# Performance work log

Hardware: AMD Instinct MI355X
Metric: run time of the kernel (lower is better)

Reference implementation:

```python
import jax, jax.numpy as jnp
import numpy as np

L, H, C, HS, V, BS = 4, 4, 1024, 256, 32000, 1024  # layers, heads, n_embd, head_size, vocab, block_size
B, T = 4, 1024
EPS = 1e-5

def _ln(x, g, b):
    mu = jnp.mean(x, axis=-1, keepdims=True)
    var = jnp.mean((x - mu) ** 2, axis=-1, keepdims=True)
    return (x - mu) / jnp.sqrt(var + EPS) * g + b

def setup_inputs() -> dict:
    key = jax.random.key(0)
    ks = iter(jax.random.split(key, 32))
    s = 0.02
    inp = {
        'idx': jax.random.randint(next(ks), (B, T), 0, V),
        'tok_emb': jax.random.normal(next(ks), (V, C), jnp.float32) * s,
        'pos_emb': jax.random.normal(next(ks), (BS, C), jnp.float32) * s,
        'wq': jax.random.normal(next(ks), (L, H, C, HS), jnp.float32) * s,
        'wk': jax.random.normal(next(ks), (L, H, C, HS), jnp.float32) * s,
        'wv': jax.random.normal(next(ks), (L, H, C, HS), jnp.float32) * s,
        'proj_w': jax.random.normal(next(ks), (L, C, C), jnp.float32) * s,
        'proj_b': jnp.zeros((L, C), jnp.float32),
        'ln1_g': jnp.ones((L, C), jnp.float32),
        'ln1_b': jnp.zeros((L, C), jnp.float32),
        'ln2_g': jnp.ones((L, C), jnp.float32),
        'ln2_b': jnp.zeros((L, C), jnp.float32),
        'ff_w1': jax.random.normal(next(ks), (L, C, 4 * C), jnp.float32) * s,
        'ff_b1': jnp.zeros((L, 4 * C), jnp.float32),
        'ff_w2': jax.random.normal(next(ks), (L, 4 * C, C), jnp.float32) * s,
        'ff_b2': jnp.zeros((L, C), jnp.float32),
        'lnf_g': jnp.ones((C,), jnp.float32),
        'lnf_b': jnp.zeros((C,), jnp.float32),
        'head_w': jax.random.normal(next(ks), (C, V), jnp.float32) * s,
        'head_b': jnp.zeros((V,), jnp.float32),
    }
    return inp

def reference(idx, tok_emb, pos_emb, wq, wk, wv, proj_w, proj_b, ln1_g, ln1_b,
              ln2_g, ln2_b, ff_w1, ff_b1, ff_w2, ff_b2, lnf_g, lnf_b, head_w, head_b):
    b, t = idx.shape
    x = tok_emb[idx] + pos_emb[:t]  # (B,T,C)
    causal = jnp.tril(jnp.ones((t, t), bool))
    inv_sqrt_c = np.float32(1.0 / np.sqrt(C))  # NOTE: original scales by sqrt(n_embd), not head_size
    for l in range(L):
        xn = _ln(x, ln1_g[l], ln1_b[l])
        q = jnp.einsum('btc,hcd->bhtd', xn, wq[l])
        k = jnp.einsum('bsc,hcd->bhsd', xn, wk[l])
        v = jnp.einsum('bsc,hcd->bhsd', xn, wv[l])
        scores = jnp.einsum('bhtd,bhsd->bhts', q, k)
        scores = jnp.where(causal, scores, -jnp.inf) * inv_sqrt_c
        # original: F.softmax(xdot, dim=1) on (B,T,T) -> normalize over the QUERY axis
        alpha = jax.nn.softmax(scores, axis=2)
        y = jnp.einsum('bhts,bhsd->bhtd', alpha, v)
        y = y.transpose(0, 2, 1, 3).reshape(b, t, C)  # concat heads
        x = x + y @ proj_w[l] + proj_b[l]
        xn2 = _ln(x, ln2_g[l], ln2_b[l])
        h = jax.nn.relu(xn2 @ ff_w1[l] + ff_b1[l])
        x = x + h @ ff_w2[l] + ff_b2[l]
    x = _ln(x, lnf_g, lnf_b)
    logits = x @ head_w + head_b  # (B,T,V)
    return logits
```

## Files before the change

### kernel.cpp

```cpp
#include <hip/hip_runtime.h>


#define C_  1024
#define T_  1024
#define HS_ 256
#define H_  4
#define L_  4
#define V_  32000
#define B_  4
#define M_  4096

typedef __attribute__((ext_vector_type(8))) short  bfx8;
typedef __attribute__((ext_vector_type(4))) float  fx4;
typedef __attribute__((ext_vector_type(4))) unsigned short usx4;

__device__ __forceinline__ unsigned short f2bf(float f) {
  unsigned int u = __builtin_bit_cast(unsigned int, f);
  u += 0x7fffu + ((u >> 16) & 1u);
  return (unsigned short)(u >> 16);
}
__device__ __forceinline__ float bf2f(unsigned short u) {
  return __builtin_bit_cast(float, ((unsigned int)u) << 16);
}

__device__ __forceinline__ void gload16(const unsigned short* g, unsigned short* l) {
  __builtin_amdgcn_global_load_lds(
      (const __attribute__((address_space(1))) unsigned int*)g,
      (__attribute__((address_space(3))) unsigned int*)l, 16, 0, 0);
}

template<int BIAS, int RES, int RELU, int OUTBF>
__global__ __launch_bounds__(256, 2) void gemm_bf16(
    const unsigned short* __restrict__ A, const unsigned short* __restrict__ Bm,
    const float* __restrict__ bias, const float* __restrict__ res,
    void* __restrict__ out,
    int M, int N, int K, int lda, int ldb, int ldc,
    long sA, long sB, long sC1, long sC2, int zShift, long rowOuter)
{
  __shared__ unsigned short As[128 * 32];
  __shared__ unsigned short Bs[128 * 32];
  const int z = blockIdx.z;
  A  += (long)z * sA;
  Bm += (long)z * sB;
  const long outOff = ((long)(z >> zShift)) * sC1 + (long)(z & ((1 << zShift) - 1)) * sC2;
  const int m0 = blockIdx.x * 128, n0 = blockIdx.y * 128;
  const int tid = threadIdx.x;
  const int lane = tid & 63, wave = tid >> 6;
  const int wm = (wave >> 1) * 64, wn = (wave & 1) * 64;
  const int fr = lane & 15, kb = lane >> 4;
  const int sr = lane >> 2;
  const int csw = (((lane & 3) ^ ((lane >> 3) & 3)) << 3);
  const int aco = ((kb ^ ((lane >> 1) & 3)) << 3);

  fx4 acc[4][4] = {};

  for (int k0 = 0; k0 < K; k0 += 32) {
    #pragma unroll
    for (int i = 0; i < 2; ++i) {
      const int c = wave * 2 + i;
      gload16(A  + (long)(m0 + c * 16 + sr) * lda + k0 + csw, &As[c * 512]);
      gload16(Bm + (long)(n0 + c * 16 + sr) * ldb + k0 + csw, &Bs[c * 512]);
    }
    __syncthreads();
    bfx8 af[4], bf[4];
    #pragma unroll
    for (int i = 0; i < 4; ++i)
      af[i] = *reinterpret_cast<const bfx8*>(&As[(wm + i * 16 + fr) * 32 + aco]);
    #pragma unroll
    for (int j = 0; j < 4; ++j)
      bf[j] = *reinterpret_cast<const bfx8*>(&Bs[(wn + j * 16 + fr) * 32 + aco]);
    #pragma unroll
    for (int i = 0; i < 4; ++i)
      #pragma unroll
      for (int j = 0; j < 4; ++j)
        acc[i][j] = __builtin_amdgcn_mfma_f32_16x16x32_bf16(af[i], bf[j], acc[i][j], 0, 0, 0);
    __syncthreads();
  }

  const float* resp = res;
  if (RES) resp += outOff;
  const int rbase = (lane >> 4) * 4;
  #pragma unroll
  for (int j = 0; j < 4; ++j) {
    const int n = n0 + wn + j * 16 + fr;
    float bv = 0.f;
    if (BIAS) bv = bias[n];
    #pragma unroll
    for (int i = 0; i < 4; ++i) {
      #pragma unroll
      for (int r = 0; r < 4; ++r) {
        const int m = m0 + wm + i * 16 + rbase + r;
        const long off = outOff + ((long)(m >> 10)) * rowOuter + (long)(m & 1023) * ldc + n;
        float val = acc[i][j][r] + bv;
        if (RELU) val = fmaxf(val, 0.f);
        if (RES) val += resp[((long)(m >> 10)) * rowOuter + (long)(m & 1023) * ldc + n];
        if (OUTBF) ((unsigned short*)out)[off] = f2bf(val);
        else       ((float*)out)[off] = val;
      }
    }
  }
}

#define BAR() __builtin_amdgcn_s_barrier()
#define LGKM() { asm volatile("s_waitcnt lgkmcnt(0)" ::: "memory"); \
                 __builtin_amdgcn_sched_barrier(0); }
#define VM8()  asm volatile("s_waitcnt vmcnt(8)" ::: "memory")
#define STA(tau, kh) { const int tc = (tau) < NT ? (tau) : NT - 1; \
  const unsigned short* src = A + (long)(m0 + wave * 16 + srow) * lda + tc * 64 + (kh) * 32 + csw; \
  unsigned short* d = &S[(((tau) & 1) * 2 + (kh)) * 8192 + wave * 512]; \
  gload16(src, d); gload16(src + (long)128 * lda, d + 4096); }
#define STB(tau, kh) { const int tc = (tau) < NT ? (tau) : NT - 1; \
  const unsigned short* src = Bm + (long)(n0 + wave * 16 + srow) * ldb + tc * 64 + (kh) * 32 + csw; \
  unsigned short* d = &S[32768 + (((tau) & 1) * 2 + (kh)) * 8192 + wave * 512]; \
  gload16(src, d); gload16(src + (long)128 * ldb, d + 4096); }
#define RDA(dst, par, kh, rh) { _Pragma("unroll") for (int i = 0; i < 4; ++i) \
  dst[i] = *reinterpret_cast<const bfx8*>(&S[((par)*2+(kh))*8192 + (wr*128 + (rh)*64 + i*16 + fr)*32 + aco]); }
#define RDB(dst, par, kh) { _Pragma("unroll") for (int j = 0; j < 4; ++j) \
  dst[j] = *reinterpret_cast<const bfx8*>(&S[32768 + ((par)*2+(kh))*8192 + (wc*64 + j*16 + fr)*32 + aco]); }
#define MM(rh, afx, bfx) { __builtin_amdgcn_s_setprio(1); \
  _Pragma("unroll") for (int i = 0; i < 4; ++i) { _Pragma("unroll") for (int j = 0; j < 4; ++j) \
    acc[(rh)*4+i][j] = __builtin_amdgcn_mfma_f32_16x16x32_bf16(afx[i], bfx[j], acc[(rh)*4+i][j], 0, 0, 0); } \
  __builtin_amdgcn_s_setprio(0); }

template<int BIAS, int RELU, int OUTBF, int EPI>
__global__ __launch_bounds__(512, 2) void gemm256(
    const unsigned short* __restrict__ A, const unsigned short* __restrict__ Bm,
    const float* __restrict__ bias, void* __restrict__ out,
    int K, int lda, int ldb, int ldc,
    long sA, long sB, long sC1, long rowOuter)
{
  __shared__ unsigned short S[65536];
  const int z = blockIdx.z;
  A  += (long)z * sA;
  Bm += (long)z * sB;
  const long outOff = (long)z * sC1;
  const int m0 = blockIdx.x * 256, n0 = blockIdx.y * 256;
  const int tid = threadIdx.x;
  const int lane = tid & 63, wave = tid >> 6;
  const int wr = wave >> 2, wc = wave & 3;
  const int fr = lane & 15, kb = lane >> 4;
  const int srow = lane >> 2;
  const int csw = (((lane & 3) ^ (((lane >> 5) & 1) << 1)) << 3);
  const int aco = ((kb ^ (((fr >> 3) & 1) << 1)) << 3);
  const int NT = K >> 6;
  const int NI = NT >> 1;

  fx4 acc[8][4] = {};
  bfx8 afa[4], afb[4], bf0[4], bf1[4];

  STB(0, 0); STA(0, 0); STB(0, 1); STA(0, 1);
  STB(1, 0); STA(1, 0); STB(1, 1); STA(1, 1);
  VM8();
  BAR();
  RDA(afa, 0, 0, 0); RDB(bf1, 0, 0);
  LGKM();
  BAR();

  for (int t = 0; t < NI; ++t) {
    const int u = 2 * t;
    STB(u + 2, 0); RDA(afb, 0, 0, 1);                 MM(0, afa, bf1); LGKM(); BAR();
    STA(u + 2, 0); RDA(afa, 0, 1, 0); RDB(bf0, 0, 1); MM(1, afb, bf1); LGKM(); VM8(); BAR();
    STB(u + 2, 1); RDA(afb, 0, 1, 1);                 MM(0, afa, bf0); LGKM(); BAR();
    STA(u + 2, 1); RDA(afa, 1, 0, 0); RDB(bf1, 1, 0); MM(1, afb, bf0); LGKM(); VM8(); BAR();
    STB(u + 3, 0); RDA(afb, 1, 0, 1);                 MM(0, afa, bf1); LGKM(); BAR();
    STA(u + 3, 0); RDA(afa, 1, 1, 0); RDB(bf0, 1, 1); MM(1, afb, bf1); LGKM(); VM8(); BAR();
    STB(u + 3, 1); RDA(afb, 1, 1, 1);                 MM(0, afa, bf0); LGKM(); BAR();
    STA(u + 3, 1); RDA(afa, 0, 0, 0); RDB(bf1, 0, 0); MM(1, afb, bf0); LGKM(); VM8(); BAR();
  }
  asm volatile("s_waitcnt vmcnt(0)" ::: "memory");
  BAR();

  const int rbase = (lane >> 4) * 4;
  if (EPI == 1) {
    const int sel = n0 >> 10, h = (n0 >> 8) & 3;
    unsigned short* dst = (unsigned short*)out
        + (long)sel * ((long)B_ * H_ * T_ * HS_) + (long)h * T_ * HS_;
    #pragma unroll
    for (int j = 0; j < 4; ++j) {
      const int d = wc * 64 + j * 16 + fr;
      #pragma unroll
      for (int i = 0; i < 8; ++i) {
        #pragma unroll
        for (int r = 0; r < 4; ++r) {
          const int m = m0 + wr * 128 + i * 16 + rbase + r;
          const int bq = m >> 10, tq = m & 1023;
          dst[(long)bq * H_ * T_ * HS_ + (long)tq * HS_ + d] = f2bf(acc[i][j][r]);
        }
      }
    }
  } else {
    float* lf = (float*)S;
    #pragma unroll
    for (int jh = 0; jh < 2; ++jh) {
      #pragma unroll
      for (int jj = 0; jj < 2; ++jj)
        #pragma unroll
        for (int i = 0; i < 8; ++i)
          #pragma unroll
          for (int r = 0; r < 4; ++r) {
            const int row = i * 16 + rbase + r;
            const int cw = (jj * 16 + fr) ^ ((row & 7) << 2);
            lf[wave * 4096 + row * 32 + cw] = acc[i][jh * 2 + jj][r];
          }
      #pragma unroll
      for (int rs = 0; rs < 16; ++rs) {
        const int row = rs * 8 + (lane >> 3);
        const int c0 = (lane & 7) * 4;
        const int cw = c0 ^ ((row & 7) << 2);
        fx4 val = *reinterpret_cast<const fx4*>(&lf[wave * 4096 + row * 32 + cw]);
        const int n = n0 + wc * 64 + jh * 32 + c0;
        const int m = m0 + wr * 128 + row;
        const long off = outOff + ((long)(m >> 10)) * rowOuter + (long)(m & 1023) * ldc + n;
        if (BIAS) {
          const float4 bb = *reinterpret_cast<const float4*>(bias + n);
          val[0] += bb.x; val[1] += bb.y; val[2] += bb.z; val[3] += bb.w;
        }
        if (RELU) {
          val[0] = fmaxf(val[0], 0.f); val[1] = fmaxf(val[1], 0.f);
          val[2] = fmaxf(val[2], 0.f); val[3] = fmaxf(val[3], 0.f);
        }
        if (OUTBF) {
          usx4 o = { f2bf(val[0]), f2bf(val[1]), f2bf(val[2]), f2bf(val[3]) };
          *reinterpret_cast<usx4*>((unsigned short*)out + off) = o;
        } else {
          *reinterpret_cast<float4*>((float*)out + off) = *(const float4*)&val;
        }
      }
      __builtin_amdgcn_sched_barrier(0);
    }
  }
}

template<typename TIN>
__global__ __launch_bounds__(256) void transpose_k(const TIN* __restrict__ src,
    unsigned short* __restrict__ dst, int R, int Cc, int zShiftT, long sOuter) {
  __shared__ float ts[64][65];
  const long zb = blockIdx.z;
  src += zb * (long)R * Cc;
  dst += (zb >> zShiftT) * sOuter + (zb & ((1 << zShiftT) - 1)) * ((long)R * Cc);
  const int r0 = blockIdx.y * 64, c0 = blockIdx.x * 64;
  const int tr = threadIdx.x >> 4;
  const int tc = (threadIdx.x & 15) * 4;
  #pragma unroll
  for (int it = 0; it < 4; ++it) {
    const int r = tr + it * 16;
    float4 v;
    if constexpr (sizeof(TIN) == 4) {
      v = *reinterpret_cast<const float4*>(src + (long)(r0 + r) * Cc + c0 + tc);
    } else {
      usx4 u = *reinterpret_cast<const usx4*>(src + (long)(r0 + r) * Cc + c0 + tc);
      v.x = bf2f(u[0]); v.y = bf2f(u[1]); v.z = bf2f(u[2]); v.w = bf2f(u[3]);
    }
    ts[r][tc + 0] = v.x; ts[r][tc + 1] = v.y; ts[r][tc + 2] = v.z; ts[r][tc + 3] = v.w;
  }
  __syncthreads();
  #pragma unroll
  for (int it = 0; it < 4; ++it) {
    const int cj = tr + it * 16;
    usx4 o = { f2bf(ts[tc + 0][cj]), f2bf(ts[tc + 1][cj]),
               f2bf(ts[tc + 2][cj]), f2bf(ts[tc + 3][cj]) };
    *reinterpret_cast<usx4*>(dst + (long)(c0 + cj) * R + r0 + tc) = o;
  }
}

__global__ __launch_bounds__(256) void embed_k(const int* __restrict__ idx,
                                               const float* __restrict__ tok,
                                               const float* __restrict__ pos,
                                               float* __restrict__ x) {
  const int row = blockIdx.x;
  const int t = row & (T_ - 1);
  const int id = idx[row];
  const int c = threadIdx.x * 4;
  const float4 a = *reinterpret_cast<const float4*>(tok + (long)id * C_ + c);
  const float4 p = *reinterpret_cast<const float4*>(pos + (long)t * C_ + c);
  float4 ov = { a.x + p.x, a.y + p.y, a.z + p.z, a.w + p.w };
  *reinterpret_cast<float4*>(x + (long)row * C_ + c) = ov;
}

__global__ __launch_bounds__(256) void ln_k(const float* __restrict__ x,
                                            const float* __restrict__ g,
                                            const float* __restrict__ b,
                                            unsigned short* __restrict__ o) {
  __shared__ float red[8];
  const int row = blockIdx.x;
  const int c = threadIdx.x * 4;
  const float4 v = *reinterpret_cast<const float4*>(x + (long)row * C_ + c);
  float s1 = v.x + v.y + v.z + v.w;
  float s2 = v.x * v.x + v.y * v.y + v.z * v.z + v.w * v.w;
  #pragma unroll
  for (int off = 32; off; off >>= 1) {
    s1 += __shfl_xor(s1, off, 64);
    s2 += __shfl_xor(s2, off, 64);
  }
  const int lane = threadIdx.x & 63, w = threadIdx.x >> 6;
  if (lane == 0) { red[w] = s1; red[4 + w] = s2; }
  __syncthreads();
  s1 = red[0] + red[1] + red[2] + red[3];
  s2 = red[4] + red[5] + red[6] + red[7];
  const float mu = s1 * (1.f / C_);
  float var = s2 * (1.f / C_) - mu * mu;
  var = fmaxf(var, 0.f);
  const float inv = rsqrtf(var + 1e-5f);
  const float4 gg = *reinterpret_cast<const float4*>(g + c);
  const float4 bb = *reinterpret_cast<const float4*>(b + c);
  usx4 ov;
  ov[0] = f2bf((v.x - mu) * inv * gg.x + bb.x);
  ov[1] = f2bf((v.y - mu) * inv * gg.y + bb.y);
  ov[2] = f2bf((v.z - mu) * inv * gg.z + bb.z);
  ov[3] = f2bf((v.w - mu) * inv * gg.w + bb.w);
  *reinterpret_cast<usx4*>(o + (long)row * C_ + c) = ov;
}

__global__ __launch_bounds__(256) void colsm_k(const unsigned short* __restrict__ a,
                                               unsigned short* __restrict__ aT) {
  __shared__ float red[8];
  const int row = blockIdx.x;
  const int s = row & (T_ - 1);
  const unsigned short* p = a + (long)row * T_;
  const int t0 = threadIdx.x * 4;
  const usx4 u = *reinterpret_cast<const usx4*>(p + t0);
  const float scale = 0.03125f;
  float vals[4];
  float m = -1e30f;
  #pragma unroll
  for (int j = 0; j < 4; ++j) {
    vals[j] = (t0 + j >= s) ? bf2f(u[j]) * scale : -1e30f;
    m = fmaxf(m, vals[j]);
  }
  #pragma unroll
  for (int off = 32; off; off >>= 1) m = fmaxf(m, __shfl_xor(m, off, 64));
  const int lane = threadIdx.x & 63, w = threadIdx.x >> 6;
  if (lane == 0) red[w] = m;
  __syncthreads();
  m = fmaxf(fmaxf(red[0], red[1]), fmaxf(red[2], red[3]));
  __syncthreads();
  float e[4], sum = 0.f;
  #pragma unroll
  for (int j = 0; j < 4; ++j) {
    e[j] = (t0 + j >= s) ? __expf(vals[j] - m) : 0.f;
    sum += e[j];
  }
  #pragma unroll
  for (int off = 32; off; off >>= 1) sum += __shfl_xor(sum, off, 64);
  if (lane == 0) red[w] = sum;
  __syncthreads();
  sum = red[0] + red[1] + red[2] + red[3];
  const float inv = 1.f / sum;
  usx4 ov = { f2bf(e[0] * inv), f2bf(e[1] * inv), f2bf(e[2] * inv), f2bf(e[3] * inv) };
  *reinterpret_cast<usx4*>(aT + (long)row * T_ + t0) = ov;
}

extern "C" void kernel_launch(void* const* d_in, const int* in_sizes, int n_in,
                              void* d_out, int out_size, void* d_ws, size_t ws_size,
                              hipStream_t stream) {
  const int*   idx    = (const int*)d_in[0];
  const float* tok    = (const float*)d_in[1];
  const float* pos    = (const float*)d_in[2];
  const float* wq     = (const float*)d_in[3];
  const float* wk     = (const float*)d_in[4];
  const float* wv     = (const float*)d_in[5];
  const float* proj_w = (const float*)d_in[6];
  const float* proj_b = (const float*)d_in[7];
  const float* ln1_g  = (const float*)d_in[8];
  const float* ln1_b  = (const float*)d_in[9];
  const float* ln2_g  = (const float*)d_in[10];
  const float* ln2_b  = (const float*)d_in[11];
  const float* ff_w1  = (const float*)d_in[12];
  const float* ff_b1  = (const float*)d_in[13];
  const float* ff_w2  = (const float*)d_in[14];
  const float* ff_b2  = (const float*)d_in[15];
  const float* lnf_g  = (const float*)d_in[16];
  const float* lnf_b  = (const float*)d_in[17];
  const float* head_w = (const float*)d_in[18];
  const float* head_b = (const float*)d_in[19];
  float* outp = (float*)d_out;

  typedef unsigned short us;
  char* w = (char*)d_ws;
  float* x    = (float*)(w + 0);
  us* xn      = (us*)(w + 16777216);
  us* qkv     = (us*)(w + 25165824);
  us* kptr    = qkv + 4194304;
  us* vptr    = qkv + 8388608;
  us* vT      = (us*)(w + 50331648);
  us* yc      = (us*)(w + 58720256);
  us* sc      = (us*)(w + 67108864);
  us* headT   = (us*)(w + 67108864);
  us* alpha   = (us*)(w + 100663296);
  us* aT      = (us*)(w + 134217728);
  us* hidden  = aT;
  us* wqkvT   = (us*)(w + 167772160);
  us* projT   = (us*)(w + 192937984);
  us* ff1T    = (us*)(w + 201326592);
  us* ff2T    = (us*)(w + 234881024);
  if (ws_size < (size_t)268435456) return;

  const long HHC = (long)H_ * HS_ * C_;
  transpose_k<float><<<dim3(HS_/64, C_/64, L_*H_), 256, 0, stream>>>(wq, wqkvT,           C_, HS_, 2, 3*HHC);
  transpose_k<float><<<dim3(HS_/64, C_/64, L_*H_), 256, 0, stream>>>(wk, wqkvT + HHC,     C_, HS_, 2, 3*HHC);
  transpose_k<float><<<dim3(HS_/64, C_/64, L_*H_), 256, 0, stream>>>(wv, wqkvT + 2*HHC,   C_, HS_, 2, 3*HHC);
  transpose_k<float><<<dim3(C_/64, C_/64, L_), 256, 0, stream>>>(proj_w, projT, C_, C_, 0, (long)C_*C_);
  transpose_k<float><<<dim3(4*C_/64, C_/64, L_), 256, 0, stream>>>(ff_w1, ff1T, C_, 4*C_, 0, (long)C_*4*C_);
  transpose_k<float><<<dim3(C_/64, 4*C_/64, L_), 256, 0, stream>>>(ff_w2, ff2T, 4*C_, C_, 0, (long)4*C_*C_);

  embed_k<<<M_, 256, 0, stream>>>(idx, tok, pos, x);

  for (int l = 0; l < L_; ++l) {
    ln_k<<<M_, 256, 0, stream>>>(x, ln1_g + l * C_, ln1_b + l * C_, xn);

    dim3 gqkv(M_/256, 3*C_/256, 1);
    gemm256<0,0,1,1><<<gqkv, 512, 0, stream>>>(xn, wqkvT + l * 3 * HHC, nullptr, qkv,
        C_, C_, C_, 0, 0, 0, 0, 0);

    dim3 gs(T_/256, T_/256, B_*H_);
    gemm256<0,0,1,0><<<gs, 512, 0, stream>>>(kptr, qkv, nullptr, sc,
        HS_, HS_, HS_, T_, (long)T_*HS_, (long)T_*HS_, (long)T_*T_, 0);

    colsm_k<<<B_*H_*T_, 256, 0, stream>>>(sc, aT);

    transpose_k<us><<<dim3(T_/64, T_/64, B_*H_), 256, 0, stream>>>(aT, alpha, T_, T_, 0, (long)T_*T_);
    transpose_k<us><<<dim3(HS_/64, T_/64, B_*H_), 256, 0, stream>>>(vptr, vT, T_, HS_, 0, (long)T_*HS_);

    dim3 gp(T_/128, HS_/128, B_*H_);
    gemm_bf16<0,0,0,1><<<gp, 256, 0, stream>>>(alpha, vT, nullptr, nullptr, yc,
        T_, HS_, T_, T_, T_, C_, (long)T_*T_, (long)HS_*T_, (long)T_*C_, HS_, 2, (long)T_*C_);

    dim3 gj(M_/128, C_/128, 1);
    gemm_bf16<1,1,0,0><<<gj, 256, 0, stream>>>(yc, projT + (long)l*C_*C_, proj_b + l*C_, x, x,
        M_, C_, C_, C_, C_, C_, 0, 0, 0, 0, 0, (long)T_*C_);

    ln_k<<<M_, 256, 0, stream>>>(x, ln2_g + l * C_, ln2_b + l * C_, xn);

    dim3 g1(M_/256, 4*C_/256, 1);
    gemm256<1,1,1,0><<<g1, 512, 0, stream>>>(xn, ff1T + (long)l*4*C_*C_, ff_b1 + (long)l*4*C_,
        hidden, C_, C_, C_, 4*C_, 0, 0, 0, (long)1024*4*C_);

    dim3 g2(M_/128, C_/128, 1);
    gemm_bf16<1,1,0,0><<<g2, 256, 0, stream>>>(hidden, ff2T + (long)l*C_*4*C_, ff_b2 + l*C_, x, x,
        M_, C_, 4*C_, 4*C_, 4*C_, C_, 0, 0, 0, 0, 0, (long)T_*C_);
  }

  ln_k<<<M_, 256, 0, stream>>>(x, lnf_g, lnf_b, xn);

  transpose_k<float><<<dim3(V_/64, C_/64, 1), 256, 0, stream>>>(head_w, headT, C_, V_, 0, (long)C_*V_);

  dim3 gh(M_/256, V_/256, 1);
  gemm256<1,0,0,0><<<gh, 512, 0, stream>>>(xn, headT, head_b, outp,
      C_, C_, C_, V_, 0, 0, 0, (long)1024*V_);
}
```

Measured before the change: 1.605 ms.

## Fuse column softmax with transpose and stage QKV epilogue through LDS

```diff
diff --git a/kernel.cpp b/kernel.cpp
--- a/kernel.cpp
+++ b/kernel.cpp
@@ -13,6 +13,7 @@
 typedef __attribute__((ext_vector_type(8))) short  bfx8;
 typedef __attribute__((ext_vector_type(4))) float  fx4;
 typedef __attribute__((ext_vector_type(4))) unsigned short usx4;
+typedef __attribute__((ext_vector_type(8))) unsigned short usx8;
 
 __device__ __forceinline__ unsigned short f2bf(float f) {
   unsigned int u = __builtin_bit_cast(unsigned int, f);
@@ -126,8 +127,7 @@
 __global__ __launch_bounds__(512, 2) void gemm256(
     const unsigned short* __restrict__ A, const unsigned short* __restrict__ Bm,
     const float* __restrict__ bias, void* __restrict__ out,
-    int K, int lda, int ldb, int ldc,
-    long sA, long sB, long sC1, long rowOuter)
+    int K, int lda, int ldb, int ldc, long sA, long sB, long sC1)
 {
   __shared__ unsigned short S[65536];
   const int z = blockIdx.z;
@@ -171,63 +171,56 @@
   BAR();
 
   const int rbase = (lane >> 4) * 4;
+  unsigned short* dst1 = nullptr;
   if (EPI == 1) {
     const int sel = n0 >> 10, h = (n0 >> 8) & 3;
-    unsigned short* dst = (unsigned short*)out
-        + (long)sel * ((long)B_ * H_ * T_ * HS_) + (long)h * T_ * HS_;
-    #pragma unroll
-    for (int j = 0; j < 4; ++j) {
-      const int d = wc * 64 + j * 16 + fr;
+    const int bq = m0 >> 10, tq0 = m0 & 1023;
+    dst1 = (unsigned short*)out + ((long)sel * B_ + bq) * H_ * T_ * HS_
+         + (long)h * T_ * HS_ + (long)tq0 * HS_;
+  }
+  float* lf = (float*)S;
+  #pragma unroll
+  for (int jh = 0; jh < 2; ++jh) {
+    #pragma unroll
+    for (int jj = 0; jj < 2; ++jj)
       #pragma unroll
-      for (int i = 0; i < 8; ++i) {
+      for (int i = 0; i < 8; ++i)
         #pragma unroll
         for (int r = 0; r < 4; ++r) {
-          const int m = m0 + wr * 128 + i * 16 + rbase + r;
-          const int bq = m >> 10, tq = m & 1023;
-          dst[(long)bq * H_ * T_ * HS_ + (long)tq * HS_ + d] = f2bf(acc[i][j][r]);
+          const int row = i * 16 + rbase + r;
+          const int cw = (jj * 16 + fr) ^ ((row & 7) << 2);
+          lf[wave * 4096 + row * 32 + cw] = acc[i][jh * 2 + jj][r];
         }
+    #pragma unroll
+    for (int rs = 0; rs < 16; ++rs) {
+      const int row = rs * 8 + (lane >> 3);
+      const int c0 = (lane & 7) * 4;
+      const int cw = c0 ^ ((row & 7) << 2);
+      fx4 val = *reinterpret_cast<const fx4*>(&lf[wave * 4096 + row * 32 + cw]);
+      const int nl = wc * 64 + jh * 32 + c0;
+      if (BIAS) {
+        const float4 bb = *reinterpret_cast<const float4*>(bias + n0 + nl);
+        val[0] += bb.x; val[1] += bb.y; val[2] += bb.z; val[3] += bb.w;
       }
-    }
-  } else {
-    float* lf = (float*)S;
-    #pragma unroll
-    for (int jh = 0; jh < 2; ++jh) {
-      #pragma unroll
-      for (int jj = 0; jj < 2; ++jj)
-        #pragma unroll
-        for (int i = 0; i < 8; ++i)
-          #pragma unroll
-          for (int r = 0; r < 4; ++r) {
-            const int row = i * 16 + rbase + r;
-            const int cw = (jj * 16 + fr) ^ ((row & 7) << 2);
-            lf[wave * 4096 + row * 32 + cw] = acc[i][jh * 2 + jj][r];
-          }
-      #pragma unroll
-      for (int rs = 0; rs < 16; ++rs) {
-        const int row = rs * 8 + (lane >> 3);
-        const int c0 = (lane & 7) * 4;
-        const int cw = c0 ^ ((row & 7) << 2);
-        fx4 val = *reinterpret_cast<const fx4*>(&lf[wave * 4096 + row * 32 + cw]);
-        const int n = n0 + wc * 64 + jh * 32 + c0;
-        const int m = m0 + wr * 128 + row;
-        const long off = outOff + ((long)(m >> 10)) * rowOuter + (long)(m & 1023) * ldc + n;
-        if (BIAS) {
-          const float4 bb = *reinterpret_cast<const float4*>(bias + n);
-          val[0] += bb.x; val[1] += bb.y; val[2] += bb.z; val[3] += bb.w;
-        }
-        if (RELU) {
-          val[0] = fmaxf(val[0], 0.f); val[1] = fmaxf(val[1], 0.f);
-          val[2] = fmaxf(val[2], 0.f); val[3] = fmaxf(val[3], 0.f);
-        }
+      if (RELU) {
+        val[0] = fmaxf(val[0], 0.f); val[1] = fmaxf(val[1], 0.f);
+        val[2] = fmaxf(val[2], 0.f); val[3] = fmaxf(val[3], 0.f);
+      }
+      if (EPI == 1) {
+        const long off = (long)(wr * 128 + row) * HS_ + nl;
+        usx4 o = { f2bf(val[0]), f2bf(val[1]), f2bf(val[2]), f2bf(val[3]) };
+        *reinterpret_cast<usx4*>(dst1 + off) = o;
+      } else {
+        const long off = outOff + (long)(m0 + wr * 128 + row) * ldc + n0 + nl;
         if (OUTBF) {
           usx4 o = { f2bf(val[0]), f2bf(val[1]), f2bf(val[2]), f2bf(val[3]) };
           *reinterpret_cast<usx4*>((unsigned short*)out + off) = o;
         } else {
-          *reinterpret_cast<float4*>((float*)out + off) = *(const float4*)&val;
+          __builtin_nontemporal_store(val, reinterpret_cast<fx4*>((float*)out + off));
         }
       }
-      __builtin_amdgcn_sched_barrier(0);
-    }
+    }
+    __builtin_amdgcn_sched_barrier(0);
   }
 }
 
@@ -311,43 +304,75 @@
   *reinterpret_cast<usx4*>(o + (long)row * C_ + c) = ov;
 }
 
-__global__ __launch_bounds__(256) void colsm_k(const unsigned short* __restrict__ a,
-                                               unsigned short* __restrict__ aT) {
-  __shared__ float red[8];
-  const int row = blockIdx.x;
-  const int s = row & (T_ - 1);
-  const unsigned short* p = a + (long)row * T_;
-  const int t0 = threadIdx.x * 4;
-  const usx4 u = *reinterpret_cast<const usx4*>(p + t0);
+__global__ __launch_bounds__(256) void colsmT_k(const unsigned short* __restrict__ sc,
+                                                unsigned short* __restrict__ alpha) {
+  __shared__ float ms[64], invs[64];
+  __shared__ float tile[64][65];
+  const int z = blockIdx.z;
+  const int s0 = blockIdx.x * 64;
+  const int r = threadIdx.x >> 2;
+  const int tq = threadIdx.x & 3;
+  const int s = s0 + r;
+  const unsigned short* p = sc + (long)z * T_ * T_ + (long)s * T_ + tq * 256;
   const float scale = 0.03125f;
-  float vals[4];
+
   float m = -1e30f;
-  #pragma unroll
-  for (int j = 0; j < 4; ++j) {
-    vals[j] = (t0 + j >= s) ? bf2f(u[j]) * scale : -1e30f;
-    m = fmaxf(m, vals[j]);
-  }
-  #pragma unroll
-  for (int off = 32; off; off >>= 1) m = fmaxf(m, __shfl_xor(m, off, 64));
-  const int lane = threadIdx.x & 63, w = threadIdx.x >> 6;
-  if (lane == 0) red[w] = m;
+  for (int i = 0; i < 32; ++i) {
+    const usx8 u = *reinterpret_cast<const usx8*>(p + i * 8);
+    #pragma unroll
+    for (int j = 0; j < 8; ++j) {
+      const int t = tq * 256 + i * 8 + j;
+      if (t >= s) m = fmaxf(m, bf2f(u[j]) * scale);
+    }
+  }
+  m = fmaxf(m, __shfl_xor(m, 1, 64));
+  m = fmaxf(m, __shfl_xor(m, 2, 64));
+  if (tq == 0) ms[r] = m;
   __syncthreads();
-  m = fmaxf(fmaxf(red[0], red[1]), fmaxf(red[2], red[3]));
+  m = ms[r];
+
+  float zsum = 0.f;
+  for (int i = 0; i < 32; ++i) {
+    const usx8 u = *reinterpret_cast<const usx8*>(p + i * 8);
+    #pragma unroll
+    for (int j = 0; j < 8; ++j) {
+      const int t = tq * 256 + i * 8 + j;
+      if (t >= s) zsum += __expf(bf2f(u[j]) * scale - m);
+    }
+  }
+  zsum += __shfl_xor(zsum, 1, 64);
+  zsum += __shfl_xor(zsum, 2, 64);
+  if (tq == 0) invs[r] = 1.f / zsum;
   __syncthreads();
-  float e[4], sum = 0.f;
-  #pragma unroll
-  for (int j = 0; j < 4; ++j) {
-    e[j] = (t0 + j >= s) ? __expf(vals[j] - m) : 0.f;
-    sum += e[j];
-  }
-  #pragma unroll
-  for (int off = 32; off; off >>= 1) sum += __shfl_xor(sum, off, 64);
-  if (lane == 0) red[w] = sum;
-  __syncthreads();
-  sum = red[0] + red[1] + red[2] + red[3];
-  const float inv = 1.f / sum;
-  usx4 ov = { f2bf(e[0] * inv), f2bf(e[1] * inv), f2bf(e[2] * inv), f2bf(e[3] * inv) };
-  *reinterpret_cast<usx4*>(aT + (long)row * T_ + t0) = ov;
+  const float inv = invs[r];
+
+  const unsigned short* prow = sc + (long)z * T_ * T_ + (long)s * T_;
+  unsigned short* ob = alpha + (long)z * T_ * T_ + s0;
+  const int wrow = threadIdx.x >> 2;
+  const int seg  = threadIdx.x & 3;
+  for (int tc = 0; tc < 16; ++tc) {
+    #pragma unroll
+    for (int half = 0; half < 2; ++half) {
+      const int tb = tc * 64 + tq * 16 + half * 8;
+      const usx8 u = *reinterpret_cast<const usx8*>(prow + tb);
+      #pragma unroll
+      for (int j = 0; j < 8; ++j) {
+        const int t = tb + j;
+        const float a = (t >= s) ? __expf(bf2f(u[j]) * scale - m) * inv : 0.f;
+        tile[tq * 16 + half * 8 + j][r] = a;
+      }
+    }
+    __syncthreads();
+    usx8 o0, o1;
+    #pragma unroll
+    for (int k = 0; k < 8; ++k) o0[k] = f2bf(tile[wrow][seg * 16 + k]);
+    #pragma unroll
+    for (int k = 0; k < 8; ++k) o1[k] = f2bf(tile[wrow][seg * 16 + 8 + k]);
+    unsigned short* od = ob + (long)(tc * 64 + wrow) * T_ + seg * 16;
+    *reinterpret_cast<usx8*>(od) = o0;
+    *reinterpret_cast<usx8*>(od + 8) = o1;
+    __syncthreads();
+  }
 }
 
 extern "C" void kernel_launch(void* const* d_in, const int* in_sizes, int n_in,
@@ -387,8 +412,7 @@
   us* sc      = (us*)(w + 67108864);
   us* headT   = (us*)(w + 67108864);
   us* alpha   = (us*)(w + 100663296);
-  us* aT      = (us*)(w + 134217728);
-  us* hidden  = aT;
+  us* hidden  = (us*)(w + 134217728);
   us* wqkvT   = (us*)(w + 167772160);
   us* projT   = (us*)(w + 192937984);
   us* ff1T    = (us*)(w + 201326592);
@@ -410,15 +434,14 @@
 
     dim3 gqkv(M_/256, 3*C_/256, 1);
     gemm256<0,0,1,1><<<gqkv, 512, 0, stream>>>(xn, wqkvT + l * 3 * HHC, nullptr, qkv,
-        C_, C_, C_, 0, 0, 0, 0, 0);
+        C_, C_, C_, 0, 0, 0, 0);
 
     dim3 gs(T_/256, T_/256, B_*H_);
     gemm256<0,0,1,0><<<gs, 512, 0, stream>>>(kptr, qkv, nullptr, sc,
-        HS_, HS_, HS_, T_, (long)T_*HS_, (long)T_*HS_, (long)T_*T_, 0);
-
-    colsm_k<<<B_*H_*T_, 256, 0, stream>>>(sc, aT);
-
-    transpose_k<us><<<dim3(T_/64, T_/64, B_*H_), 256, 0, stream>>>(aT, alpha, T_, T_, 0, (long)T_*T_);
+        HS_, HS_, HS_, T_, (long)T_*HS_, (long)T_*HS_, (long)T_*T_);
+
+    colsmT_k<<<dim3(T_/64, 1, B_*H_), 256, 0, stream>>>(sc, alpha);
+
     transpose_k<us><<<dim3(HS_/64, T_/64, B_*H_), 256, 0, stream>>>(vptr, vT, T_, HS_, 0, (long)T_*HS_);
 
     dim3 gp(T_/128, HS_/128, B_*H_);
@@ -433,7 +456,7 @@
 
     dim3 g1(M_/256, 4*C_/256, 1);
     gemm256<1,1,1,0><<<g1, 512, 0, stream>>>(xn, ff1T + (long)l*4*C_*C_, ff_b1 + (long)l*4*C_,
-        hidden, C_, C_, C_, 4*C_, 0, 0, 0, (long)1024*4*C_);
+        hidden, C_, C_, C_, 4*C_, 0, 0, 0);
 
     dim3 g2(M_/128, C_/128, 1);
     gemm_bf16<1,1,0,0><<<g2, 256, 0, stream>>>(hidden, ff2T + (long)l*C_*4*C_, ff_b2 + l*C_, x, x,
@@ -446,5 +469,5 @@
 
   dim3 gh(M_/256, V_/256, 1);
   gemm256<1,0,0,0><<<gh, 512, 0, stream>>>(xn, headT, head_b, outp,
-      C_, C_, C_, V_, 0, 0, 0, (long)1024*V_);
-}
+      C_, C_, C_, V_, 0, 0, 0);
+}
```

After: 1.561 ms. -2.7%, faster.
